# Optimization experiments

Measured on AMD Instinct MI355X. Metric: run time of the kernel, lower is better.

The kernel has to match this reference:

```python
import jax, jax.numpy as jnp
import numpy as np

LAM = 0.7      # lambda_param
GAM = 2.0      # gamma (weight upper bound)
ALPHA = 0.1    # age modulation scale
FGAM = 0.1     # fusion_gamma
SIGMAS = jnp.array([0.1, 0.5, 1.0, 2.0], dtype=jnp.float32)  # multi-kernel sigmas


def setup_inputs() -> dict:
    key = jax.random.key(0)
    ks = jax.random.split(key, 12)
    B, C, D, H, W, K = 12, 64, 32, 32, 32, 32
    mid, red = C // 2, C // 4
    Z = jax.random.normal(ks[0], (B, C, D, H, W), jnp.float32)
    masks = (jax.random.uniform(ks[1], (K, D, H, W)) > 0.5).astype(jnp.float32)
    masks = masks.at[:, 0, 0, 0].set(1.0)  # guarantee every region non-empty
    labels = jnp.arange(B, dtype=jnp.int32) % 3  # 4 samples each of CN/MCI/AD
    ages = 50.0 + 40.0 * jax.random.uniform(ks[2], (B,), jnp.float32)
    prior_weights = 1.0 + 0.1 * jax.random.normal(ks[3], (K,), jnp.float32)
    struct_w = 0.05 * jax.random.normal(ks[4], (mid, C), jnp.float32)
    noise_w = 0.05 * jax.random.normal(ks[5], (mid, C), jnp.float32)
    up_w = 0.05 * jax.random.normal(ks[6], (C, mid), jnp.float32)
    region_w = 0.05 * jax.random.normal(ks[7], (C, C, 3, 3, 3), jnp.float32)
    m_w1 = 0.05 * jax.random.normal(ks[8], (red, C), jnp.float32)
    m_b1 = jnp.zeros((red,), jnp.float32)
    m_w2 = 0.05 * jax.random.normal(ks[9], (C, red), jnp.float32)
    m_b2 = jnp.zeros((C,), jnp.float32)
    return dict(Z=Z, masks=masks, labels=labels, ages=ages, prior_weights=prior_weights,
                struct_w=struct_w, noise_w=noise_w, up_w=up_w, region_w=region_w,
                m_w1=m_w1, m_b1=m_b1, m_w2=m_w2, m_b2=m_b2)


def _mmd_pair(kern, ca, cb):
    # kern: [S,K,B,B] RBF kernels; ca/cb: [B] float class indicators.
    # Unbiased MMD^2 per region, averaged over sigmas -> [K].
    m = ca.sum()
    n = cb.sum()
    Kaa = jnp.einsum('skij,i,j->sk', kern, ca, ca)
    da = jnp.einsum('skii,i->sk', kern, ca)
    Kbb = jnp.einsum('skij,i,j->sk', kern, cb, cb)
    db = jnp.einsum('skii,i->sk', kern, cb)
    t1 = (Kaa - da) / (m * (m - 1.0))
    t2 = (Kbb - db) / (n * (n - 1.0))
    t3 = jnp.einsum('skij,i,j->sk', kern, ca, cb) * (-2.0 / (m * n))
    return (t1 + t2 + t3).mean(0)


def _forward(Z, masks, labels, ages, prior_weights, struct_w, noise_w, up_w,
             region_w, m_w1, m_b1, m_w2, m_b2):
    B, C = Z.shape[:2]
    K = masks.shape[0]
    # --- region-specific aggregation (fused segment-reduce over masks) ---
    msum = masks.sum((1, 2, 3))                                   # [K]
    rf = jnp.einsum('bcdhw,kdhw->bkc', Z, masks) / (msum[None, :, None] + 1e-6)
    # --- multi-class multi-kernel MMD per region ---
    x2 = jnp.sum(rf * rf, -1)                                     # [B,K]
    ip = jnp.einsum('ikc,jkc->kij', rf, rf)                       # [K,B,B]
    d2 = jnp.maximum(x2.T[:, :, None] + x2.T[:, None, :] - 2.0 * ip, 0.0)
    kern = jnp.exp(-d2[None] / (2.0 * SIGMAS[:, None, None, None] ** 2))  # [S,K,B,B]
    c_cn = (labels == 0).astype(jnp.float32)
    c_mci = (labels == 1).astype(jnp.float32)
    c_ad = (labels == 2).astype(jnp.float32)
    D_mmd = (_mmd_pair(kern, c_ad, c_cn) + _mmd_pair(kern, c_mci, c_cn)
             + _mmd_pair(kern, c_ad, c_mci))                      # [K]
    max_mmd = jnp.maximum(D_mmd.max(), 1e-6)
    nm = jnp.clip(D_mmd / max_mmd, 0.0)
    # symmetric KL between prior and MMD-evidence distributions (batchmean -> /K)
    lp = jax.nn.log_softmax(prior_weights)
    lq = jax.nn.log_softmax(nm)
    p = jnp.exp(lp)
    q = jnp.exp(lq)
    reg = 0.5 * jnp.sum(q * (lq - lp)) / K + 0.5 * jnp.sum(p * (lp - lq)) / K
    # --- prior-guided adaptive spatial weights ---
    base = LAM * prior_weights + (1.0 - LAM) * nm
    af = 1.0 + jax.nn.softplus(ALPHA * (ages - 50.0))             # [B]
    Wk = jax.nn.softmax(jnp.clip(base[None, :] * af[:, None], 0.0, GAM), axis=1)
    spatial = jnp.einsum('bk,kdhw->bdhw', Wk, masks)[:, None]     # [B,1,D,H,W]
    # --- orthogonal decomposition ---
    cs = jnp.einsum('oc,bcdhw->bodhw', struct_w, Z)               # 1x1x1 conv
    cnoise = jnp.einsum('oc,bcdhw->bodhw', noise_w, Z)
    s = cs.reshape(B, cs.shape[1], -1)
    n = cnoise.reshape(B, cnoise.shape[1], -1)
    eps = 1e-8
    cos = jnp.sum(s * n, -1) / (jnp.maximum(jnp.linalg.norm(s, axis=-1), eps)
                                * jnp.maximum(jnp.linalg.norm(n, axis=-1), eps))
    ortho = jnp.abs(cos).mean()
    Z_clean = jnp.einsum('oc,bcdhw->bodhw', up_w, cs)
    # --- region base field + 3x3x3 conv + channel modulation ---
    Zrb = jnp.einsum('bkc,kdhw->bcdhw', rf, masks)
    Zrec = jax.lax.conv_general_dilated(
        Zrb, region_w, (1, 1, 1), 'SAME',
        dimension_numbers=('NCDHW', 'OIDHW', 'NCDHW'))
    h = jax.nn.relu(jnp.einsum('bkc,rc->bkr', rf, m_w1) + m_b1)
    mod = jax.nn.softplus(jnp.einsum('bkr,cr->bkc', h, m_w2) + m_b2)  # [B,K,C]
    Zmod = Zrec * jnp.einsum('bkc,kdhw->bcdhw', mod, masks)
    Z_out = Z_clean + FGAM * (Zmod * spatial)
    return rf, spatial, Z_out, reg + ortho


def reference(Z, masks, labels, ages, prior_weights, struct_w, noise_w, up_w,
              region_w, m_w1, m_b1, m_w2, m_b2):
    return _forward(Z, masks, labels, ages, prior_weights, struct_w, noise_w,
                    up_w, region_w, m_w1, m_b1, m_w2, m_b2)
```

## Files before the change

### kernel.cpp

```cpp
#include <hip/hip_runtime.h>
#include <hip/hip_bf16.h>
#include <math.h>

#define REG_OFF    0
#define ORTHO_OFF  1
#define FLAG_OFF   2
#define MSUM_OFF   4
#define RF_OFF     64
#define G_OFF      24640
#define WKW_OFF    73792
#define MODTB_OFF  74176
#define M1TTH_OFF  86464
#define M1TTL_OFF  88512
#define WKCB_OFF   90560
#define IPK_OFF    422336
#define WS_TOTAL   426944
#define ZERO_FLOATS 73792

#define RF_OUT   0
#define SPAT_OUT 24576
#define ZOUT_OUT 417792
#define SCAL_OUT 25583616

typedef unsigned short u16;
typedef short bh8 __attribute__((ext_vector_type(8)));
typedef float fv4 __attribute__((ext_vector_type(4)));

__device__ __forceinline__ float bf2f(u16 u) {
  union { unsigned int i; float f; } x; x.i = ((unsigned int)u) << 16; return x.f;
}
__device__ __forceinline__ u16 f2bf(float f) {
  unsigned int u = __float_as_uint(f);
  return (u16)((u + 0x7fffu + ((u >> 16) & 1u)) >> 16);
}
__device__ __forceinline__ float ldin(const void* p, size_t i, bool f32) {
  return f32 ? ((const float*)p)[i] : bf2f(((const u16*)p)[i]);
}

__global__ void k_probe(const void* __restrict__ Z, float* __restrict__ ws) {
  int t = threadIdx.x;
  const u16* s = (const u16*)Z;
  float mx = 0.f;
  for (int i = t; i < 8192; i += 256) {
    float a = fabsf(bf2f(s[i]));
    if (!(a < 1e30f)) a = 3e38f;
    mx = fmaxf(mx, a);
  }
  __shared__ float r[256];
  r[t] = mx; __syncthreads();
  for (int o = 128; o > 0; o >>= 1) { if (t < o) r[t] = fmaxf(r[t], r[t + o]); __syncthreads(); }
  if (t == 0) ws[FLAG_OFF] = (r[0] > 1e6f) ? 1.f : 0.f;
}

__global__ void k_msum(const void* __restrict__ masks, float* __restrict__ ws) {
  int k = blockIdx.x, t = threadIdx.x;
  bool f32 = ws[FLAG_OFF] > 0.5f;
  float s = 0.f;
  for (int v = t; v < 32768; v += 256) s += ldin(masks, ((size_t)k << 15) + v, f32);
  __shared__ float red[256];
  red[t] = s; __syncthreads();
  for (int off = 128; off > 0; off >>= 1) { if (t < off) red[t] += red[t + off]; __syncthreads(); }
  if (t == 0) ws[MSUM_OFF + k] = red[0];
}

__global__ __launch_bounds__(256) void k_rfgram(const void* __restrict__ Z,
                                                const void* __restrict__ masks,
                                                float* __restrict__ ws) {
  __shared__ float Zt[64][68];
  __shared__ float Mt[64][36];
  int b = blockIdx.y, t = threadIdx.x;
  bool f32 = ws[FLAG_OFF] > 0.5f;
  int ci = t & 15, gj = t >> 4;
  int c0 = ci << 2, c20 = gj << 2, k0 = gj << 1;
  float accG[16], accR[8];
#pragma unroll
  for (int i = 0; i < 16; i++) accG[i] = 0.f;
#pragma unroll
  for (int i = 0; i < 8; i++) accR[i] = 0.f;
  int vs = blockIdx.x << 9;
  for (int t8 = 0; t8 < 8; t8++) {
    int vb = vs + (t8 << 6);
    __syncthreads();
    if (f32) {
      const float* Zf = (const float*)Z;
      const float* Mf = (const float*)masks;
#pragma unroll
      for (int i = 0; i < 8; i++) {
        int idx = (i << 8) + t, c = idx >> 5, v2 = (idx & 31) << 1;
        float2 u = *(const float2*)(Zf + (((size_t)(b << 6) + c) << 15) + vb + v2);
        Zt[v2][c] = u.x; Zt[v2 + 1][c] = u.y;
      }
#pragma unroll
      for (int i = 0; i < 4; i++) {
        int idx = (i << 8) + t, k = idx >> 5, v2 = (idx & 31) << 1;
        float2 u = *(const float2*)(Mf + ((size_t)k << 15) + vb + v2);
        Mt[v2][k] = u.x; Mt[v2 + 1][k] = u.y;
      }
    } else {
      const u16* Zs = (const u16*)Z;
      const u16* Ms = (const u16*)masks;
#pragma unroll
      for (int i = 0; i < 8; i++) {
        int idx = (i << 8) + t, c = idx >> 5, v2 = (idx & 31) << 1;
        unsigned int u = *(const unsigned int*)(Zs + (((size_t)(b << 6) + c) << 15) + vb + v2);
        Zt[v2][c]     = bf2f((u16)(u & 0xffff));
        Zt[v2 + 1][c] = bf2f((u16)(u >> 16));
      }
#pragma unroll
      for (int i = 0; i < 4; i++) {
        int idx = (i << 8) + t, k = idx >> 5, v2 = (idx & 31) << 1;
        unsigned int u = *(const unsigned int*)(Ms + ((size_t)k << 15) + vb + v2);
        Mt[v2][k]     = bf2f((u16)(u & 0xffff));
        Mt[v2 + 1][k] = bf2f((u16)(u >> 16));
      }
    }
    __syncthreads();
    for (int vt = 0; vt < 64; vt++) {
      float4 z1 = *(const float4*)&Zt[vt][c0];
      float4 z2 = *(const float4*)&Zt[vt][c20];
      float2 m2 = *(const float2*)&Mt[vt][k0];
      float z1a[4] = {z1.x, z1.y, z1.z, z1.w};
      float z2a[4] = {z2.x, z2.y, z2.z, z2.w};
      float m2a[2] = {m2.x, m2.y};
#pragma unroll
      for (int i = 0; i < 4; i++) {
#pragma unroll
        for (int j = 0; j < 4; j++) accG[(i << 2) + j] += z1a[i] * z2a[j];
#pragma unroll
        for (int kk = 0; kk < 2; kk++) accR[(i << 1) + kk] += z1a[i] * m2a[kk];
      }
    }
  }
  float* Gd = ws + G_OFF + (b << 12);
  float* Rd = ws + RF_OFF + (b << 11);
#pragma unroll
  for (int i = 0; i < 4; i++) {
#pragma unroll
    for (int j = 0; j < 4; j++) atomicAdd(Gd + ((c0 + i) << 6) + c20 + j, accG[(i << 2) + j]);
#pragma unroll
    for (int kk = 0; kk < 2; kk++) atomicAdd(Rd + ((k0 + kk) << 6) + c0 + i, accR[(i << 1) + kk]);
  }
}

__global__ void k_scale_rf(float* __restrict__ ws, float* __restrict__ out) {
  int i = blockIdx.x * 256 + threadIdx.x;
  int k = (i >> 6) & 31;
  float v = ws[RF_OFF + i] / (ws[MSUM_OFF + k] + 1e-6f);
  ws[RF_OFF + i] = v;
  out[RF_OUT + i] = v;
}

__global__ void k_ipk(float* __restrict__ ws) {
  __shared__ float rfk[12][65];
  int k = blockIdx.x, t = threadIdx.x;
  for (int i = t; i < 768; i += 256) {
    int b = i >> 6, c = i & 63;
    rfk[b][c] = ws[RF_OFF + (((size_t)(b << 5) + k) << 6) + c];
  }
  __syncthreads();
  if (t < 144) {
    int i = t / 12, j = t - (t / 12) * 12;
    float s = 0.f;
#pragma unroll
    for (int c = 0; c < 64; c++) s += rfk[i][c] * rfk[j][c];
    ws[IPK_OFF + k * 144 + t] = s;
  }
}

__global__ void k_mmdw(const int* __restrict__ labels, const void* __restrict__ ages,
                       const void* __restrict__ prior, float* __restrict__ ws) {
  __shared__ float IPL[32 * 145];
  __shared__ float dpart[128];
  __shared__ float Dm[32], nms[32], bases[32], pwl[32];
  __shared__ int labs[12];
  int t = threadIdx.x;
  bool f32 = ws[FLAG_OFF] > 0.5f;
  if (t < 12) labs[t] = labels[t];
  for (int i = t; i < 4608; i += 256) {
    int k = i / 144, r = i - k * 144;
    IPL[k * 145 + r] = ws[IPK_OFF + i];
  }
  __syncthreads();
  if (t < 128) {
    int k = t >> 2, s = t & 3;
    const float inv2s2[4] = {50.f, 2.f, 0.5f, 0.125f};
    float inv = inv2s2[s];
    const float* pk = IPL + k * 145;
    float c0 = 0.f, c1 = 0.f, c2 = 0.f;
#pragma unroll
    for (int i = 0; i < 12; i++) {
      int li = labs[i];
      c0 += (li == 0) ? 1.f : 0.f;
      c1 += (li == 1) ? 1.f : 0.f;
      c2 += (li == 2) ? 1.f : 0.f;
    }
    float s00=0,s01=0,s02=0,s10=0,s11=0,s12=0,s20=0,s21=0,s22=0;
    float dg0=0, dg1=0, dg2=0;
    for (int i = 0; i < 12; i++) {
      int li = labs[i];
      float x2i = pk[i * 13];
      float r0=0, r1=0, r2=0, dge=0;
      for (int j = 0; j < 12; j++) {
        float d2 = fmaxf(x2i + pk[j * 13] - 2.f * pk[i * 12 + j], 0.f);
        float e = expf(-d2 * inv);
        int lj = labs[j];
        r0 += (lj == 0) ? e : 0.f;
        r1 += (lj == 1) ? e : 0.f;
        r2 += (lj == 2) ? e : 0.f;
        if (j == i) dge = e;
      }
      if (li == 0)      { s00 += r0; s01 += r1; s02 += r2; dg0 += dge; }
      else if (li == 1) { s10 += r0; s11 += r1; s12 += r2; dg1 += dge; }
      else              { s20 += r0; s21 += r1; s22 += r2; dg2 += dge; }
    }
    float ta = (s22 - dg2) / (c2 * (c2 - 1.f));
    float tb = (s00 - dg0) / (c0 * (c0 - 1.f));
    float tc = (s11 - dg1) / (c1 * (c1 - 1.f));
    float dsum = (ta + tb - 2.f * s20 / (c2 * c0))
               + (tc + tb - 2.f * s10 / (c1 * c0))
               + (ta + tc - 2.f * s21 / (c2 * c1));
    dpart[t] = dsum;
  }
  __syncthreads();
  if (t < 32) {
    Dm[t] = (dpart[t * 4] + dpart[t * 4 + 1] + dpart[t * 4 + 2] + dpart[t * 4 + 3]) * 0.25f;
    pwl[t] = (float)ldin(prior, t, f32);
  }
  __syncthreads();
  if (t == 0) {
    float mx = 1e-6f;
    for (int k = 0; k < 32; k++) mx = fmaxf(mx, Dm[k]);
    float nmax = -1e30f, pmax = -1e30f;
    for (int k = 0; k < 32; k++) {
      nms[k] = fmaxf(Dm[k] / mx, 0.f);
      nmax = fmaxf(nmax, nms[k]);
      pmax = fmaxf(pmax, pwl[k]);
    }
    float nse = 0.f, pse = 0.f;
    for (int k = 0; k < 32; k++) { nse += expf(nms[k] - nmax); pse += expf(pwl[k] - pmax); }
    float lns = logf(nse), lps = logf(pse);
    float reg = 0.f;
    for (int k = 0; k < 32; k++) {
      float lqk = nms[k] - nmax - lns;
      float lpk = pwl[k] - pmax - lps;
      reg += 0.5f * (expf(lqk) * (lqk - lpk) + expf(lpk) * (lpk - lqk));
    }
    ws[REG_OFF] = reg / 32.f;
    for (int k = 0; k < 32; k++) bases[k] = 0.7f * pwl[k] + 0.3f * nms[k];
  }
  __syncthreads();
  if (t < 12) {
    float x = 0.1f * (ldin(ages, t, f32) - 50.f);
    float af = 1.f + fmaxf(x, 0.f) + log1pf(expf(-fabsf(x)));
    float w[32];
    float mx = -1e30f;
#pragma unroll
    for (int k = 0; k < 32; k++) {
      float v = fminf(fmaxf(bases[k] * af, 0.f), 2.f);
      w[k] = v; mx = fmaxf(mx, v);
    }
    float se = 0.f;
#pragma unroll
    for (int k = 0; k < 32; k++) se += expf(w[k] - mx);
#pragma unroll
    for (int k = 0; k < 32; k++) ws[WKW_OFF + (t << 5) + k] = expf(w[k] - mx) / se;
  }
}

__global__ __launch_bounds__(64) void k_mod(const void* __restrict__ m_w1, const void* __restrict__ m_b1,
                                            const void* __restrict__ m_w2, const void* __restrict__ m_b2,
                                            float* __restrict__ ws) {
  __shared__ float W1[16][65];
  __shared__ float W2T[16][64];
  __shared__ float B1[16], B2[64], RL[64], H[16];
  int bk = blockIdx.x, t = threadIdx.x;
  int bb = bk >> 5, kk = bk & 31;
  bool f32 = ws[FLAG_OFF] > 0.5f;
  for (int i = t; i < 1024; i += 64) {
    W1[i >> 6][i & 63] = ldin(m_w1, i, f32);
    W2T[i & 15][i >> 4] = ldin(m_w2, i, f32);
  }
  if (t < 16) B1[t] = ldin(m_b1, t, f32);
  B2[t] = ldin(m_b2, t, f32);
  RL[t] = ws[RF_OFF + (bk << 6) + t];
  __syncthreads();
  if (t < 16) {
    float s = B1[t];
#pragma unroll
    for (int c = 0; c < 64; c++) s += RL[c] * W1[t][c];
    H[t] = fmaxf(s, 0.f);
  }
  __syncthreads();
  {
    int c = t;
    float s = B2[c];
#pragma unroll
    for (int rr = 0; rr < 16; rr++) s += H[rr] * W2T[rr][c];
    float mv = fmaxf(s, 0.f) + log1pf(expf(-fabsf(s)));
    ((u16*)(ws + MODTB_OFF))[((size_t)bb * 64 + c) * 32 + kk] = f2bf(mv);
  }
}

__global__ void k_m1t(const void* __restrict__ struct_w, const void* __restrict__ up_w,
                      float* __restrict__ ws) {
  __shared__ float UPT[32][64];
  __shared__ float ST[32][64];
  int t = threadIdx.x, blk = blockIdx.x;
  bool f32 = ws[FLAG_OFF] > 0.5f;
  for (int i = t; i < 2048; i += 256) {
    UPT[i & 31][i >> 5] = ldin(up_w, i, f32);
    ST[i >> 6][i & 63] = ldin(struct_w, i, f32);
  }
  __syncthreads();
  int idx = (blk << 8) + t;
  int cin = idx >> 6, co = idx & 63;
  float s = 0.f;
#pragma unroll
  for (int j = 0; j < 32; j++) s += UPT[j][co] * ST[j][cin];
  u16 hi = f2bf(s);
  ((u16*)(ws + M1TTH_OFF))[co * 64 + cin] = hi;
  ((u16*)(ws + M1TTL_OFF))[co * 64 + cin] = f2bf(s - bf2f(hi));
}

__global__ void k_ortho(const void* __restrict__ sw, const void* __restrict__ nw,
                        float* __restrict__ ws) {
  int b = blockIdx.x >> 5, o = blockIdx.x & 31, c = threadIdx.x;
  bool f32 = ws[FLAG_OFF] > 0.5f;
  const float* Gb = ws + G_OFF + (b << 12);
  float ts = 0.f, tn = 0.f;
  for (int c2 = 0; c2 < 64; c2++) {
    float g = Gb[(c << 6) + c2];
    ts += g * ldin(sw, (o << 6) + c2, f32);
    tn += g * ldin(nw, (o << 6) + c2, f32);
  }
  float swc = ldin(sw, (o << 6) + c, f32);
  float nwc = ldin(nw, (o << 6) + c, f32);
  float ds = swc * tn, ss = swc * ts, nn = nwc * tn;
  for (int off = 32; off > 0; off >>= 1) {
    ds += __shfl_down(ds, off);
    ss += __shfl_down(ss, off);
    nn += __shfl_down(nn, off);
  }
  if (c == 0) {
    ss = fmaxf(ss, 0.f); nn = fmaxf(nn, 0.f);
    float cosv = ds / (fmaxf(sqrtf(ss), 1e-8f) * fmaxf(sqrtf(nn), 1e-8f));
    atomicAdd(ws + ORTHO_OFF, fabsf(cosv) * (1.f / 384.f));
  }
}

__global__ void k_wk(const void* __restrict__ rw, float* __restrict__ ws) {
  int bk = blockIdx.x;
  int b = bk >> 5, k = bk & 31;
  int t = threadIdx.x;
  bool f32 = ws[FLAG_OFF] > 0.5f;
  __shared__ float rl[64];
  if (t < 64) rl[t] = ws[RF_OFF + (bk << 6) + t];
  __syncthreads();
  u16* dst = (u16*)(ws + WKCB_OFF);
  for (int idx = t; idx < 1728; idx += 256) {
    int o = idx / 27, d = idx - o * 27;
    float s = 0.f;
    for (int c = 0; c < 64; c++) s += rl[c] * ldin(rw, (size_t)o * 1728 + c * 27 + d, f32);
    dst[(((size_t)b * 64 + o) * 27 + d) * 32 + k] = f2bf(s);
  }
}

__global__ void k_spatial(const void* __restrict__ masks, const float* __restrict__ ws,
                          float* __restrict__ out) {
  int b = blockIdx.y, t = threadIdx.x;
  bool f32 = ws[FLAG_OFF] > 0.5f;
  __shared__ float wl[32];
  if (t < 32) wl[t] = ws[WKW_OFF + (b << 5) + t];
  __syncthreads();
  int v0 = (blockIdx.x << 11) + (t << 3);
  float s[8] = {0, 0, 0, 0, 0, 0, 0, 0};
  for (int k = 0; k < 32; k++) {
    float wkv = wl[k];
    float mv[8];
    if (f32) {
      const float* Mf = (const float*)masks + ((size_t)k << 15) + v0;
      float4 a = *(const float4*)Mf, bb = *(const float4*)(Mf + 4);
      mv[0]=a.x; mv[1]=a.y; mv[2]=a.z; mv[3]=a.w; mv[4]=bb.x; mv[5]=bb.y; mv[6]=bb.z; mv[7]=bb.w;
    } else {
      uint4 u = *(const uint4*)((const u16*)masks + ((size_t)k << 15) + v0);
      mv[0]=bf2f((u16)(u.x & 0xffff)); mv[1]=bf2f((u16)(u.x >> 16));
      mv[2]=bf2f((u16)(u.y & 0xffff)); mv[3]=bf2f((u16)(u.y >> 16));
      mv[4]=bf2f((u16)(u.z & 0xffff)); mv[5]=bf2f((u16)(u.z >> 16));
      mv[6]=bf2f((u16)(u.w & 0xffff)); mv[7]=bf2f((u16)(u.w >> 16));
    }
#pragma unroll
    for (int j = 0; j < 8; j++) s[j] += wkv * mv[j];
  }
#pragma unroll
  for (int j = 0; j < 8; j++) out[SPAT_OUT + (b << 15) + v0 + j] = s[j];
}

#define MHS 40
__global__ __launch_bounds__(256, 3) void k_final(const void* __restrict__ Z,
                                                  const void* __restrict__ masks,
                                                  const float* __restrict__ ws,
                                                  float* __restrict__ out) {
  __shared__ u16 POOL[24000];
  __shared__ float wl[32];
  __shared__ float spl[256];
  u16* MHT = POOL;
  u16* ZTH = POOL;
  u16* ZTL = POOL + 8192;

  int b = blockIdx.y, tile = blockIdx.x, t = threadIdx.x;
  int lane = t & 63, w = t >> 6;
  int lo16 = lane & 15, g = lane >> 4, g8 = g << 3;
  bool f32 = ws[FLAG_OFF] > 0.5f;
  int d0 = (tile >> 4) << 2, h0 = ((tile >> 2) & 3) << 3, w0 = (tile & 3) << 3;

  for (int i = t; i < 32 * 600; i += 256) {
    int k = i / 600, r = i - k * 600;
    int hd = r / 100, rr = r - hd * 100, hh = rr / 10, hw = rr - hh * 10;
    int gd = d0 - 1 + hd, gh = h0 - 1 + hh, gw = w0 - 1 + hw;
    u16 val = 0;
    if ((unsigned)gd < 32u && (unsigned)gh < 32u && (unsigned)gw < 32u) {
      float mv = ldin(masks, ((size_t)k << 15) + (gd << 10) + (gh << 5) + gw, f32);
      val = (u16)(__float_as_uint(mv) >> 16);
    }
    MHT[r * MHS + k] = val;
  }
  if (t < 32) wl[t] = ws[WKW_OFF + (b << 5) + t];
  __syncthreads();

  {
    int dz = t >> 6, hy = (t >> 3) & 7, wx = t & 7;
    const u16* cen = MHT + (dz * 100 + hy * 10 + wx + 111) * MHS;
    float sp = 0.f;
#pragma unroll
    for (int k = 0; k < 32; k++) sp += wl[k] * bf2f(cen[k]);
    spl[t] = sp;
  }

  int hb4[4], v4[4];
#pragma unroll
  for (int pt = 0; pt < 4; pt++) {
    int pos = (w << 6) + (pt << 4) + lo16;
    int dz = pos >> 6, hy = (pos >> 3) & 7, wx = pos & 7;
    hb4[pt] = dz * 100 + hy * 10 + wx;
    v4[pt] = ((d0 + dz) << 10) + ((h0 + hy) << 5) + (w0 + wx);
  }

  fv4 acc[4][4];
#pragma unroll
  for (int ot = 0; ot < 4; ot++)
#pragma unroll
    for (int pt = 0; pt < 4; pt++) { acc[ot][pt][0]=0.f; acc[ot][pt][1]=0.f; acc[ot][pt][2]=0.f; acc[ot][pt][3]=0.f; }

  const u16* Wb = (const u16*)(ws + WKCB_OFF) + (size_t)b * 55296;
#pragma unroll 3
  for (int d = 0; d < 27; d++) {
    int da = d / 9, r9 = d - da * 9, db = r9 / 3, dc = r9 - db * 3;
    int off = da * 100 + db * 10 + dc;
    bh8 a[4];
#pragma unroll
    for (int ot = 0; ot < 4; ot++)
      a[ot] = *(const bh8*)(Wb + ((ot << 4) + lo16) * 864 + (d << 5) + g8);
#pragma unroll
    for (int pt = 0; pt < 4; pt++) {
      bh8 bv = *(const bh8*)(MHT + (hb4[pt] + off) * MHS + g8);
#pragma unroll
      for (int ot = 0; ot < 4; ot++)
        acc[ot][pt] = __builtin_amdgcn_mfma_f32_16x16x32_bf16(a[ot], bv, acc[ot][pt], 0, 0, 0);
    }
  }

  {
    const u16* modtb = (const u16*)(ws + MODTB_OFF);
    bh8 am[4];
#pragma unroll
    for (int ot = 0; ot < 4; ot++)
      am[ot] = *(const bh8*)(modtb + ((size_t)b * 64 + (ot << 4) + lo16) * 32 + g8);
    fv4 zero4; zero4[0]=0.f; zero4[1]=0.f; zero4[2]=0.f; zero4[3]=0.f;
#pragma unroll
    for (int pt = 0; pt < 4; pt++) {
      bh8 bc = *(const bh8*)(MHT + (hb4[pt] + 111) * MHS + g8);
      float spf = 0.1f * spl[(w << 6) + (pt << 4) + lo16];
#pragma unroll
      for (int ot = 0; ot < 4; ot++) {
        fv4 mm = __builtin_amdgcn_mfma_f32_16x16x32_bf16(am[ot], bc, zero4, 0, 0, 0);
        acc[ot][pt] = acc[ot][pt] * mm * spf;
      }
    }
  }

  const u16* m1tth = (const u16*)(ws + M1TTH_OFF);
  const u16* m1ttl = (const u16*)(ws + M1TTL_OFF);
  int dzs = t >> 6, hys = (t >> 3) & 7, wxs = t & 7;
  int vstage = ((d0 + dzs) << 10) + ((h0 + hys) << 5) + (w0 + wxs);
#pragma unroll 1
  for (int st = 0; st < 2; st++) {
    int cb = st << 5;
    __syncthreads();
#pragma unroll
    for (int gg = 0; gg < 4; gg++) {
      bh8 hb, lb;
#pragma unroll
      for (int j = 0; j < 8; j++) {
        int c = cb + (gg << 3) + j;
        float zv = ldin(Z, (((size_t)(b << 6) + c) << 15) + vstage, f32);
        u16 h = f2bf(zv);
        hb[j] = (short)h;
        lb[j] = (short)f2bf(zv - bf2f(h));
      }
      *(bh8*)(ZTH + (((gg << 8) + t) << 3)) = hb;
      *(bh8*)(ZTL + (((gg << 8) + t) << 3)) = lb;
    }
    __syncthreads();
    bh8 ah[4], al[4];
#pragma unroll
    for (int ot = 0; ot < 4; ot++) {
      ah[ot] = *(const bh8*)(m1tth + ((ot << 4) + lo16) * 64 + cb + g8);
      al[ot] = *(const bh8*)(m1ttl + ((ot << 4) + lo16) * 64 + cb + g8);
    }
#pragma unroll
    for (int pt = 0; pt < 4; pt++) {
      int pcol = (w << 6) + (pt << 4) + lo16;
      bh8 bh = *(const bh8*)(ZTH + (((g << 8) + pcol) << 3));
      bh8 bl = *(const bh8*)(ZTL + (((g << 8) + pcol) << 3));
#pragma unroll
      for (int ot = 0; ot < 4; ot++) {
        acc[ot][pt] = __builtin_amdgcn_mfma_f32_16x16x32_bf16(ah[ot], bh, acc[ot][pt], 0, 0, 0);
        acc[ot][pt] = __builtin_amdgcn_mfma_f32_16x16x32_bf16(ah[ot], bl, acc[ot][pt], 0, 0, 0);
        acc[ot][pt] = __builtin_amdgcn_mfma_f32_16x16x32_bf16(al[ot], bh, acc[ot][pt], 0, 0, 0);
      }
    }
  }

#pragma unroll
  for (int ot = 0; ot < 4; ot++)
#pragma unroll
    for (int pt = 0; pt < 4; pt++)
#pragma unroll
      for (int r = 0; r < 4; r++) {
        int o = (ot << 4) + (g << 2) + r;
        out[(size_t)ZOUT_OUT + (((size_t)(b << 6) + o) << 15) + v4[pt]] = acc[ot][pt][r];
      }
  if ((t | tile | b) == 0) out[SCAL_OUT] = ws[REG_OFF] + ws[ORTHO_OFF];
}

extern "C" void kernel_launch(void* const* d_in, const int* in_sizes, int n_in,
                              void* d_out, int out_size, void* d_ws, size_t ws_size,
                              hipStream_t stream) {
  (void)in_sizes; (void)n_in; (void)out_size; (void)ws_size;
  const void* Z        = d_in[0];
  const void* masks    = d_in[1];
  const int*  labels   = (const int*)d_in[2];
  const void* ages     = d_in[3];
  const void* prior    = d_in[4];
  const void* struct_w = d_in[5];
  const void* noise_w  = d_in[6];
  const void* up_w     = d_in[7];
  const void* region_w = d_in[8];
  const void* m_w1     = d_in[9];
  const void* m_b1     = d_in[10];
  const void* m_w2     = d_in[11];
  const void* m_b2     = d_in[12];
  float* ws = (float*)d_ws;
  float* out = (float*)d_out;

  hipMemsetAsync(d_ws, 0, (size_t)ZERO_FLOATS * 4, stream);
  k_probe<<<1, 256, 0, stream>>>(Z, ws);
  k_msum<<<32, 256, 0, stream>>>(masks, ws);
  k_rfgram<<<dim3(64, 12), 256, 0, stream>>>(Z, masks, ws);
  k_scale_rf<<<96, 256, 0, stream>>>(ws, out);
  k_m1t<<<16, 256, 0, stream>>>(struct_w, up_w, ws);
  k_ipk<<<32, 256, 0, stream>>>(ws);
  k_mmdw<<<1, 256, 0, stream>>>(labels, ages, prior, ws);
  k_mod<<<384, 64, 0, stream>>>(m_w1, m_b1, m_w2, m_b2, ws);
  k_ortho<<<384, 64, 0, stream>>>(struct_w, noise_w, ws);
  k_wk<<<384, 256, 0, stream>>>(region_w, ws);
  k_spatial<<<dim3(16, 12), 256, 0, stream>>>(masks, ws, out);
  k_final<<<dim3(128, 12), 256, 0, stream>>>(Z, masks, ws, out);
}
```

Baseline: 693.5 us.

## Bit-pack region masks in LDS and load Z directly into MFMA fragments

The final fused kernel now stores the 32 region masks as one 32-bit bitmask per halo voxel instead of a 32x40 bf16 LDS table. MFMA B fragments are rebuilt from these bits with integer ops, which shrinks LDS from about 48KB to about 3KB and lets launch bounds ask for 4 blocks per SM. The Z staging through LDS (two syncthreads per stage) is removed; each lane loads its own Z values from global memory and splits them into bf16 hi/lo. The risks are more scattered, less coalesced global Z loads, and mask values that are not exactly 0/1 being binarized.

Result: slower. 717.4 us (+3.5%).

```diff
diff --git a/kernel.cpp b/kernel.cpp
--- a/kernel.cpp
+++ b/kernel.cpp
@@ -35,6 +35,15 @@
 }
 __device__ __forceinline__ float ldin(const void* p, size_t i, bool f32) {
   return f32 ? ((const float*)p)[i] : bf2f(((const u16*)p)[i]);
+}
+__device__ __forceinline__ bh8 bits2bf8(unsigned int mbits) {
+  union { bh8 v; unsigned int w[4]; } u;
+#pragma unroll
+  for (int j = 0; j < 4; j++) {
+    unsigned int tt = mbits >> (2 * j);
+    u.w[j] = ((tt & 1u) | ((tt & 2u) << 15)) * 0x3F80u;
+  }
+  return u.v;
 }
 
 __global__ void k_probe(const void* __restrict__ Z, float* __restrict__ ws) {
@@ -395,17 +404,13 @@
   for (int j = 0; j < 8; j++) out[SPAT_OUT + (b << 15) + v0 + j] = s[j];
 }
 
-#define MHS 40
-__global__ __launch_bounds__(256, 3) void k_final(const void* __restrict__ Z,
+__global__ __launch_bounds__(256, 4) void k_final(const void* __restrict__ Z,
                                                   const void* __restrict__ masks,
                                                   const float* __restrict__ ws,
                                                   float* __restrict__ out) {
-  __shared__ u16 POOL[24000];
+  __shared__ unsigned int MHB[608];
   __shared__ float wl[32];
   __shared__ float spl[256];
-  u16* MHT = POOL;
-  u16* ZTH = POOL;
-  u16* ZTL = POOL + 8192;
 
   int b = blockIdx.y, tile = blockIdx.x, t = threadIdx.x;
   int lane = t & 63, w = t >> 6;
@@ -413,26 +418,29 @@
   bool f32 = ws[FLAG_OFF] > 0.5f;
   int d0 = (tile >> 4) << 2, h0 = ((tile >> 2) & 3) << 3, w0 = (tile & 3) << 3;
 
-  for (int i = t; i < 32 * 600; i += 256) {
-    int k = i / 600, r = i - k * 600;
+  for (int r = t; r < 600; r += 256) {
     int hd = r / 100, rr = r - hd * 100, hh = rr / 10, hw = rr - hh * 10;
     int gd = d0 - 1 + hd, gh = h0 - 1 + hh, gw = w0 - 1 + hw;
-    u16 val = 0;
+    unsigned int word = 0;
     if ((unsigned)gd < 32u && (unsigned)gh < 32u && (unsigned)gw < 32u) {
-      float mv = ldin(masks, ((size_t)k << 15) + (gd << 10) + (gh << 5) + gw, f32);
-      val = (u16)(__float_as_uint(mv) >> 16);
-    }
-    MHT[r * MHS + k] = val;
+      size_t base = (size_t)(gd << 10) + (gh << 5) + gw;
+#pragma unroll 4
+      for (int k = 0; k < 32; k++) {
+        float mv = ldin(masks, ((size_t)k << 15) + base, f32);
+        word |= (mv != 0.f ? 1u : 0u) << k;
+      }
+    }
+    MHB[r] = word;
   }
   if (t < 32) wl[t] = ws[WKW_OFF + (b << 5) + t];
   __syncthreads();
 
   {
     int dz = t >> 6, hy = (t >> 3) & 7, wx = t & 7;
-    const u16* cen = MHT + (dz * 100 + hy * 10 + wx + 111) * MHS;
+    unsigned int m = MHB[dz * 100 + hy * 10 + wx + 111];
     float sp = 0.f;
 #pragma unroll
-    for (int k = 0; k < 32; k++) sp += wl[k] * bf2f(cen[k]);
+    for (int k = 0; k < 32; k++) sp += ((m >> k) & 1u) ? wl[k] : 0.f;
     spl[t] = sp;
   }
 
@@ -462,7 +470,7 @@
       a[ot] = *(const bh8*)(Wb + ((ot << 4) + lo16) * 864 + (d << 5) + g8);
 #pragma unroll
     for (int pt = 0; pt < 4; pt++) {
-      bh8 bv = *(const bh8*)(MHT + (hb4[pt] + off) * MHS + g8);
+      bh8 bv = bits2bf8(MHB[hb4[pt] + off] >> g8);
 #pragma unroll
       for (int ot = 0; ot < 4; ot++)
         acc[ot][pt] = __builtin_amdgcn_mfma_f32_16x16x32_bf16(a[ot], bv, acc[ot][pt], 0, 0, 0);
@@ -478,7 +486,7 @@
     fv4 zero4; zero4[0]=0.f; zero4[1]=0.f; zero4[2]=0.f; zero4[3]=0.f;
 #pragma unroll
     for (int pt = 0; pt < 4; pt++) {
-      bh8 bc = *(const bh8*)(MHT + (hb4[pt] + 111) * MHS + g8);
+      bh8 bc = bits2bf8(MHB[hb4[pt] + 111] >> g8);
       float spf = 0.1f * spl[(w << 6) + (pt << 4) + lo16];
 #pragma unroll
       for (int ot = 0; ot < 4; ot++) {
@@ -488,45 +496,30 @@
     }
   }
 
-  const u16* m1tth = (const u16*)(ws + M1TTH_OFF);
-  const u16* m1ttl = (const u16*)(ws + M1TTL_OFF);
-  int dzs = t >> 6, hys = (t >> 3) & 7, wxs = t & 7;
-  int vstage = ((d0 + dzs) << 10) + ((h0 + hys) << 5) + (w0 + wxs);
+  {
+    const u16* m1tth = (const u16*)(ws + M1TTH_OFF);
+    const u16* m1ttl = (const u16*)(ws + M1TTL_OFF);
 #pragma unroll 1
-  for (int st = 0; st < 2; st++) {
-    int cb = st << 5;
-    __syncthreads();
-#pragma unroll
-    for (int gg = 0; gg < 4; gg++) {
-      bh8 hb, lb;
-#pragma unroll
-      for (int j = 0; j < 8; j++) {
-        int c = cb + (gg << 3) + j;
-        float zv = ldin(Z, (((size_t)(b << 6) + c) << 15) + vstage, f32);
-        u16 h = f2bf(zv);
-        hb[j] = (short)h;
-        lb[j] = (short)f2bf(zv - bf2f(h));
-      }
-      *(bh8*)(ZTH + (((gg << 8) + t) << 3)) = hb;
-      *(bh8*)(ZTL + (((gg << 8) + t) << 3)) = lb;
-    }
-    __syncthreads();
-    bh8 ah[4], al[4];
-#pragma unroll
-    for (int ot = 0; ot < 4; ot++) {
-      ah[ot] = *(const bh8*)(m1tth + ((ot << 4) + lo16) * 64 + cb + g8);
-      al[ot] = *(const bh8*)(m1ttl + ((ot << 4) + lo16) * 64 + cb + g8);
-    }
-#pragma unroll
-    for (int pt = 0; pt < 4; pt++) {
-      int pcol = (w << 6) + (pt << 4) + lo16;
-      bh8 bh = *(const bh8*)(ZTH + (((g << 8) + pcol) << 3));
-      bh8 bl = *(const bh8*)(ZTL + (((g << 8) + pcol) << 3));
-#pragma unroll
-      for (int ot = 0; ot < 4; ot++) {
-        acc[ot][pt] = __builtin_amdgcn_mfma_f32_16x16x32_bf16(ah[ot], bh, acc[ot][pt], 0, 0, 0);
-        acc[ot][pt] = __builtin_amdgcn_mfma_f32_16x16x32_bf16(ah[ot], bl, acc[ot][pt], 0, 0, 0);
-        acc[ot][pt] = __builtin_amdgcn_mfma_f32_16x16x32_bf16(al[ot], bh, acc[ot][pt], 0, 0, 0);
+    for (int st = 0; st < 2; st++) {
+      int cb = st << 5;
+#pragma unroll
+      for (int pt = 0; pt < 4; pt++) {
+        bh8 bh, bl;
+#pragma unroll
+        for (int j = 0; j < 8; j++) {
+          float zv = ldin(Z, (((size_t)(b << 6) + cb + g8 + j) << 15) + v4[pt], f32);
+          u16 h = f2bf(zv);
+          bh[j] = (short)h;
+          bl[j] = (short)f2bf(zv - bf2f(h));
+        }
+#pragma unroll
+        for (int ot = 0; ot < 4; ot++) {
+          bh8 ah = *(const bh8*)(m1tth + ((ot << 4) + lo16) * 64 + cb + g8);
+          bh8 al = *(const bh8*)(m1ttl + ((ot << 4) + lo16) * 64 + cb + g8);
+          acc[ot][pt] = __builtin_amdgcn_mfma_f32_16x16x32_bf16(ah, bh, acc[ot][pt], 0, 0, 0);
+          acc[ot][pt] = __builtin_amdgcn_mfma_f32_16x16x32_bf16(ah, bl, acc[ot][pt], 0, 0, 0);
+          acc[ot][pt] = __builtin_amdgcn_mfma_f32_16x16x32_bf16(al, bh, acc[ot][pt], 0, 0, 0);
+        }
       }
     }
   }
```
